# Optimization experiments

Hardware: AMD Instinct MI355X
Metric: run time of the kernel (lower is better)

## Reference

```python
import jax, jax.numpy as jnp
import numpy as np

S = 2048        # seqlen (prefill)
DIM = 4096      # model dim
NH = 32         # query heads
NKV = 8         # kv heads (GQA)
HD = 128        # head dim
SW = 4096       # sliding window / cache length
SCALE = HD ** (-0.5)
NEG = -1e9      # finite -inf for additive mask


def _rope(x, cos, sin):
    # x: (S, H, HD); cos/sin: (S, HD//2). Interleaved even/odd rotation.
    c = cos[:, None, :]
    s = sin[:, None, :]
    x1 = x[..., 0::2]
    x2 = x[..., 1::2]
    pe = jnp.stack([x1 * c - x2 * s, x1 * s + x2 * c], axis=-1)  # (S,H,HD/2,2)
    return pe.reshape(x.shape).astype(x.dtype)


def setup_inputs() -> dict:
    key = jax.random.key(0)
    kx, kq, kk, kv, ko = jax.random.split(key, 5)
    sd = 1.0 / np.sqrt(DIM)
    x = jax.random.normal(kx, (S, DIM), dtype=jnp.float32)
    wq = jax.random.normal(kq, (NH * HD, DIM), dtype=jnp.float32) * sd
    wk = jax.random.normal(kk, (NKV * HD, DIM), dtype=jnp.float32) * sd
    wv = jax.random.normal(kv, (NKV * HD, DIM), dtype=jnp.float32) * sd
    wo = jax.random.normal(ko, (DIM, NH * HD), dtype=jnp.float32) * (1.0 / np.sqrt(NH * HD))
    # RoPE tables
    inv_freq = 1.0 / (10000.0 ** (np.arange(0, HD, 2, dtype=np.float32) / HD))  # (HD/2,)
    t = np.arange(S, dtype=np.float32)
    freqs = np.outer(t, inv_freq)  # (S, HD/2)
    cos_freq = jnp.asarray(np.cos(freqs), dtype=jnp.float32)
    sin_freq = jnp.asarray(np.sin(freqs), dtype=jnp.float32)
    # sliding-window causal additive mask
    i = jnp.arange(S)[:, None]
    j = jnp.arange(S)[None, :]
    allowed = (j <= i) & ((i - j) < SW)
    mask = jnp.where(allowed, 0.0, NEG).astype(jnp.float32)
    cache_k = jnp.zeros((SW, NKV, HD), dtype=jnp.float32)
    cache_v = jnp.zeros((SW, NKV, HD), dtype=jnp.float32)
    positions = jnp.arange(S, dtype=jnp.int32)
    return {"x": x, "cos_freq": cos_freq, "sin_freq": sin_freq, "mask": mask,
            "wq": wq, "wk": wk, "wv": wv, "wo": wo,
            "cache_k": cache_k, "cache_v": cache_v, "positions": positions}


def reference(x, cos_freq, sin_freq, mask, wq, wk, wv, wo, cache_k, cache_v, positions):
    seqlen = x.shape[0]
    kv_repeats = NH // NKV
    # QKV projections (eqx.nn.Linear: y = x @ W.T)
    xq = (x @ wq.T).reshape(seqlen, NH, HD)
    xk = (x @ wk.T).reshape(seqlen, NKV, HD)
    xv = (x @ wv.T).reshape(seqlen, NKV, HD)
    # RoPE on q and k (offset 0)
    xq = _rope(xq, cos_freq, sin_freq)
    xk = _rope(xk, cos_freq, sin_freq)
    # KV-cache scatter update
    cache_k = cache_k.at[positions].set(xk[positions])
    cache_v = cache_v.at[positions].set(xv[positions])
    # prefill path: GQA head repeat
    key_ = jnp.repeat(xk, kv_repeats, axis=1)   # (S, NH, HD)
    val_ = jnp.repeat(xv, kv_repeats, axis=1)
    # explicit matmul-softmax-matmul attention, heads leading
    q = jnp.transpose(xq, (1, 0, 2))            # (NH, S, HD)
    k = jnp.transpose(key_, (1, 0, 2))
    v = jnp.transpose(val_, (1, 0, 2))
    scores = jnp.einsum('hqd,hkd->hqk', q, k) * SCALE
    scores = scores + mask[None, ...]
    probs = jax.nn.softmax(scores.astype(jnp.float32), axis=-1).astype(q.dtype)
    out = jnp.einsum('hqk,hkd->hqd', probs, v)  # (NH, S, HD)
    out = jnp.transpose(out, (1, 0, 2)).reshape(seqlen, NH * HD)
    out = out @ wo.T
    return (out, cache_k, cache_v)
```

## Files before the change

kernel.cpp:

```cpp
#include <hip/hip_runtime.h>
#include <stdint.h>

#define S_LEN 2048
#define DIM_   4096
#define NH_    32
#define NKV_   8
#define HD_    128
#define QK_SCALE 0.08838834764831845f

typedef __attribute__((ext_vector_type(8)))  short  s16x8;
typedef __attribute__((ext_vector_type(4)))  float  f32x4;
typedef __attribute__((ext_vector_type(16))) float  f32x16;
typedef __attribute__((ext_vector_type(8))) unsigned short u16x8;
typedef __attribute__((ext_vector_type(4))) unsigned short u16x4;

union frag_u { s16x8 f; uint32_t w[4]; };

__device__ __forceinline__ unsigned short f2bf(float f) {
  union { float f; uint32_t u; } v; v.f = f;
  return (unsigned short)((v.u + 0x7fffu + ((v.u >> 16) & 1u)) >> 16);
}

__device__ __forceinline__ uint32_t cvt_pk_bf16(float lo, float hi2) {
  uint32_t r;
  asm volatile("v_cvt_pk_bf16_f32 %0, %1, %2" : "=v"(r) : "v"(lo), "v"(hi2));
  return r;
}

__device__ __forceinline__ void async_cp16(const void* g, void* l) {
  __builtin_amdgcn_global_load_lds(
      (const __attribute__((address_space(1))) unsigned int*)g,
      (__attribute__((address_space(3))) unsigned int*)l, 16, 0, 0);
}

#define WAITV(n) asm volatile("s_waitcnt vmcnt(" #n ")" ::: "memory")

__global__ __launch_bounds__(256) void cast_f32_bf16(
    const float* __restrict__ src, unsigned short* __restrict__ dst, int n4) {
  const int i = blockIdx.x * 256 + threadIdx.x;
  if (i >= n4) return;
  const float4 v = ((const float4*)src)[i];
  u16x4 o; o[0] = f2bf(v.x); o[1] = f2bf(v.y); o[2] = f2bf(v.z); o[3] = f2bf(v.w);
  ((u16x4*)dst)[i] = o;
}

template <int NT, int NTILE_N, int NCF, int NBCH>
__global__ __launch_bounds__(512, 4) void gemmF(
    const unsigned short* __restrict__ A, const unsigned short* __restrict__ B,
    float* __restrict__ C, int ldc) {
  constexpr int BUFB = 16384 + NTILE_N * 128;
  __shared__ unsigned char lds[2 * BUFB];

  const int bid = blockIdx.x;
  const int idx = (bid & 7) * 64 + (bid >> 3);
  const int m = idx & 15, n = idx >> 4;
  const int m0 = m * 128, n0 = n * NTILE_N;

  const int tid = threadIdx.x;
  const int wave = tid >> 6, lane = tid & 63;
  const int wm = wave >> 2, wn = wave & 3;
  const int fr = lane & 15, g = lane >> 4;

  int offA[2][2], offB[NCF][2];
#pragma unroll
  for (int rf = 0; rf < 2; ++rf)
#pragma unroll
    for (int kk = 0; kk < 2; ++kk)
      offA[rf][kk] = (wm * 32 + rf * 16 + fr) * 128 + (((kk * 4 + g + fr) & 7) << 4);
#pragma unroll
  for (int cf = 0; cf < NCF; ++cf)
#pragma unroll
    for (int kk = 0; kk < 2; ++kk)
      offB[cf][kk] = (wn * NCF * 16 + cf * 16 + fr) * 128 + (((kk * 4 + g + fr) & 7) << 4);

  const int srk = (((tid & 7) - (tid >> 3)) & 7) * 8;
  uint32_t aoff[2];
  uint32_t boff[NBCH];
#pragma unroll
  for (int h = 0; h < 2; ++h)
    aoff[h] = (uint32_t)((m0 + h * 64 + (tid >> 3)) * 4096 + srk);
#pragma unroll
  for (int i = 0; i < NBCH; ++i)
    boff[i] = (uint32_t)((n0 + i * 64 + (tid >> 3)) * 4096 + srk);

  f32x4 acc[2][2][NCF] = {};
  s16x8 fa[2][2], fb[NCF][2];

#define STGA(H, T, BUF)                                                       \
  async_cp16(A + aoff[H] + (size_t)(T) * 64,                                  \
             (char*)lds + (BUF) * BUFB + (H) * 8192 + tid * 16);
#define STGB(T, BUF)                                                          \
  { _Pragma("unroll") for (int i_ = 0; i_ < NBCH; ++i_)                       \
      async_cp16(B + boff[i_] + (size_t)(T) * 64,                             \
                 (char*)lds + (BUF) * BUFB + 16384 + i_ * 8192 + tid * 16); }
#define LDA(AA, P)                                                            \
  { _Pragma("unroll") for (int rf = 0; rf < 2; ++rf)                          \
      _Pragma("unroll") for (int kk = 0; kk < 2; ++kk)                        \
        fa[rf][kk] = *(const s16x8*)((char*)lds + (P) * BUFB +                \
                                     (AA) * 8192 + offA[rf][kk]); }
#define LDBF(P)                                                               \
  { _Pragma("unroll") for (int cf = 0; cf < NCF; ++cf)                        \
      _Pragma("unroll") for (int kk = 0; kk < 2; ++kk)                        \
        fb[cf][kk] = *(const s16x8*)((char*)lds + (P) * BUFB + 16384 +        \
                                     offB[cf][kk]); }
#define BARLG()                                                               \
  __builtin_amdgcn_s_barrier();                                               \
  asm volatile("s_waitcnt lgkmcnt(0)" ::: "memory");                          \
  __builtin_amdgcn_sched_barrier(0);
#define MF(AA)                                                                \
  __builtin_amdgcn_s_setprio(1);                                              \
  { _Pragma("unroll") for (int kk = 0; kk < 2; ++kk)                          \
      _Pragma("unroll") for (int rf = 0; rf < 2; ++rf)                        \
        _Pragma("unroll") for (int cf = 0; cf < NCF; ++cf)                    \
          acc[AA][rf][cf] = __builtin_amdgcn_mfma_f32_16x16x32_bf16(          \
              fa[rf][kk], fb[cf][kk], acc[AA][rf][cf], 0, 0, 0); }            \
  __builtin_amdgcn_s_setprio(0);
#define GATEN do { if constexpr (NBCH == 3) { WAITV(4); } else { WAITV(3); } } while (0)

#define GROUPF(J, P, DO1, DO2, GATE)                                          \
  {                                                                           \
    LDA(0, P); LDBF(P);                                                       \
    if (DO1) { STGA(1, (J) + 1, (P) ^ 1); }                                   \
    BARLG(); MF(0);                                                           \
    __builtin_amdgcn_s_barrier();                                             \
    LDA(1, P);                                                                \
    if (DO2) { STGA(0, (J) + 2, P); STGB((J) + 2, P); }                       \
    BARLG(); MF(1);                                                           \
    GATE;                                                                     \
    __builtin_amdgcn_s_barrier();                                             \
  }

  STGA(0, 0, 0); STGB(0, 0); STGA(1, 0, 0);
  STGA(0, 1, 1); STGB(1, 1);
  GATEN;
  __builtin_amdgcn_s_barrier();

  for (int j = 0; j + 3 < NT; j += 2) {
    GROUPF(j, 0, true, true, GATEN);
    GROUPF(j + 1, 1, true, true, GATEN);
  }
  GROUPF(NT - 2, 0, true, false, WAITV(0));
  GROUPF(NT - 1, 1, false, false, );

#pragma unroll
  for (int AA = 0; AA < 2; ++AA)
#pragma unroll
    for (int rf = 0; rf < 2; ++rf)
#pragma unroll
      for (int cf = 0; cf < NCF; ++cf) {
        float* cp = C + (size_t)(m0 + AA * 64 + wm * 32 + rf * 16 + g * 4) * ldc
                      + (n0 + wn * NCF * 16 + cf * 16 + fr);
#pragma unroll
        for (int r = 0; r < 4; ++r) cp[(size_t)r * ldc] = acc[AA][rf][cf][r];
      }
#undef STGA
#undef STGB
#undef LDA
#undef LDBF
#undef BARLG
#undef MF
#undef GATEN
#undef GROUPF
}

__global__ __launch_bounds__(256) void rope_q_kern(
    const float* __restrict__ xqkv, const float* __restrict__ cos_f,
    const float* __restrict__ sin_f, unsigned short* __restrict__ qb) {
  const int gid = blockIdx.x * 256 + threadIdx.x;
  const int e0 = gid * 8;
  const int s = e0 >> 12;
  const int col = e0 & 4095;
  const int i0 = (col & 127) >> 1;
  const float* src = xqkv + (size_t)s * 6144 + col;
  const float4 f1 = *(const float4*)src;
  const float4 f2 = *(const float4*)(src + 4);
  const float4 c  = *(const float4*)(cos_f + s * 64 + i0);
  const float4 sn = *(const float4*)(sin_f + s * 64 + i0);
  u16x8 o;
  o[0] = f2bf((f1.x * c.x - f1.y * sn.x) * QK_SCALE);
  o[1] = f2bf((f1.x * sn.x + f1.y * c.x) * QK_SCALE);
  o[2] = f2bf((f1.z * c.y - f1.w * sn.y) * QK_SCALE);
  o[3] = f2bf((f1.z * sn.y + f1.w * c.y) * QK_SCALE);
  o[4] = f2bf((f2.x * c.z - f2.y * sn.z) * QK_SCALE);
  o[5] = f2bf((f2.x * sn.z + f2.y * c.z) * QK_SCALE);
  o[6] = f2bf((f2.z * c.w - f2.w * sn.w) * QK_SCALE);
  o[7] = f2bf((f2.z * sn.w + f2.w * c.w) * QK_SCALE);
  *(u16x8*)(qb + e0) = o;
}

__global__ __launch_bounds__(256) void rope_k_kern(
    const float* __restrict__ xqkv, const float* __restrict__ cos_f,
    const float* __restrict__ sin_f, float* __restrict__ ck, unsigned short* __restrict__ kb) {
  const int gid = blockIdx.x * 256 + threadIdx.x;
  const int e0 = gid * 8;
  const int s = e0 >> 10;
  const int col = e0 & 1023;
  const int i0 = (col & 127) >> 1;
  const float* src = xqkv + (size_t)s * 6144 + 4096 + col;
  const float4 f1 = *(const float4*)src;
  const float4 f2 = *(const float4*)(src + 4);
  const float4 c  = *(const float4*)(cos_f + s * 64 + i0);
  const float4 sn = *(const float4*)(sin_f + s * 64 + i0);
  const float r0 = f1.x * c.x - f1.y * sn.x, r1 = f1.x * sn.x + f1.y * c.x;
  const float r2 = f1.z * c.y - f1.w * sn.y, r3 = f1.z * sn.y + f1.w * c.y;
  const float r4 = f2.x * c.z - f2.y * sn.z, r5 = f2.x * sn.z + f2.y * c.z;
  const float r6 = f2.z * c.w - f2.w * sn.w, r7 = f2.z * sn.w + f2.w * c.w;
  float4 o1; o1.x = r0; o1.y = r1; o1.z = r2; o1.w = r3;
  float4 o2; o2.x = r4; o2.y = r5; o2.z = r6; o2.w = r7;
  *(float4*)(ck + (size_t)s * 1024 + col) = o1;
  *(float4*)(ck + (size_t)s * 1024 + col + 4) = o2;
  u16x8 o;
  o[0] = f2bf(r0); o[1] = f2bf(r1); o[2] = f2bf(r2); o[3] = f2bf(r3);
  o[4] = f2bf(r4); o[5] = f2bf(r5); o[6] = f2bf(r6); o[7] = f2bf(r7);
  *(u16x8*)(kb + (size_t)s * 1024 + col) = o;
}

__global__ __launch_bounds__(256) void vtrans_kern(
    const float* __restrict__ xqkv, float* __restrict__ cv, unsigned short* __restrict__ vtb) {
  __shared__ float tile[64][65];
  const int st = blockIdx.x * 64;
  const int ct = blockIdx.y * 64;
  const int tid = threadIdx.x;
#pragma unroll
  for (int j = 0; j < 16; ++j) {
    const int lin = tid + j * 256;
    const int si = lin >> 6, ci = lin & 63;
    const float v = xqkv[(size_t)(st + si) * 6144 + 5120 + ct + ci];
    cv[(size_t)(st + si) * 1024 + ct + ci] = v;
    tile[si][ci] = v;
  }
  __syncthreads();
#pragma unroll
  for (int j = 0; j < 16; ++j) {
    const int lin = tid + j * 256;
    const int co = lin >> 6, so = lin & 63;
    vtb[(size_t)(ct + co) * 2048 + st + so] = f2bf(tile[so][co]);
  }
}

__global__ __launch_bounds__(256, 2) void attn_fwd2(
    const unsigned short* __restrict__ qb, const unsigned short* __restrict__ kb,
    const unsigned short* __restrict__ vtb, unsigned short* __restrict__ ob) {
  __shared__ unsigned short Ks[2][64 * 128];
  __shared__ unsigned short Vs[2][128 * 64];
  const int bx = blockIdx.x;
  const int h  = blockIdx.y;
  const int hkv = h >> 2;
  const int g = (bx & 1) ? (15 - (bx >> 1)) : (bx >> 1);
  const int qtile = (h < 16) ? g : (15 - g);
  const int q0 = qtile * 128;
  const int tid = threadIdx.x, wave = tid >> 6, lane = tid & 63;
  const int col = lane & 31;
  const int hi  = lane >> 5;
  const int q0w = q0 + wave * 32;
  const int nt = (q0 >> 6) + 2;

  s16x8 qf[8];
  {
    const unsigned short* qrow = qb + (size_t)(q0w + col) * 4096 + h * 128 + hi * 8;
#pragma unroll
    for (int ks = 0; ks < 8; ++ks) qf[ks] = *(const s16x8*)(qrow + ks * 16);
  }

  f32x16 oacc[4] = {};
  float m_s = -3e30f, l_s = 0.0f;

#define STAGE_K(KT, B)                                                        \
  {                                                                           \
    const unsigned short* src = kb + (size_t)((KT) * 64) * 1024 + hkv * 128;  \
    _Pragma("unroll")                                                         \
    for (int i_ = 0; i_ < 4; ++i_) {                                          \
      const int c_ = wave * 4 + i_;                                           \
      const int row_ = c_ * 4 + (lane >> 4);                                  \
      const int cb_ = ((lane & 15) * 16) ^ ((row_ & 7) << 4);                 \
      async_cp16(src + (size_t)row_ * 1024 + (cb_ >> 1), (char*)Ks[B] + c_ * 1024); \
    }                                                                         \
  }
#define STAGE_V(KT, B)                                                        \
  {                                                                           \
    const unsigned short* src = vtb + (size_t)hkv * (128 * 2048) + (KT) * 64; \
    _Pragma("unroll")                                                         \
    for (int i_ = 0; i_ < 4; ++i_) {                                          \
      const int c_ = wave * 4 + i_;                                           \
      const int row_ = c_ * 8 + (lane >> 3);                                  \
      const int cb_ = ((lane & 7) * 16) ^ ((row_ & 7) << 4);                  \
      async_cp16(src + (size_t)row_ * 2048 + (cb_ >> 1), (char*)Vs[B] + c_ * 1024); \
    }                                                                         \
  }

  STAGE_K(0, 0); STAGE_V(0, 0);
  __syncthreads();

  for (int kt = 0; kt < nt; ++kt) {
    const int kv0 = kt * 64;
    const int cur = kt & 1;
    if (kt + 1 < nt) { STAGE_K(kt + 1, cur ^ 1); STAGE_V(kt + 1, cur ^ 1); }

    if (kv0 < q0w + 32) {
      f32x16 s0 = {}, s1 = {};
#pragma unroll
      for (int ks = 0; ks < 8; ++ks) {
        const int gcb = 32 * ks + 16 * hi;
        const int sw = (col & 7) << 4;
        const s16x8 k0 = *(const s16x8*)((const char*)Ks[cur] + col * 256 + (gcb ^ sw));
        const s16x8 k1 = *(const s16x8*)((const char*)Ks[cur] + (32 + col) * 256 + (gcb ^ sw));
        s0 = __builtin_amdgcn_mfma_f32_32x32x16_bf16(k0, qf[ks], s0, 0, 0, 0);
        s1 = __builtin_amdgcn_mfma_f32_32x32x16_bf16(k1, qf[ks], s1, 0, 0, 0);
      }

      const int qg = q0w + col;
      if (kv0 + 63 > q0w) {
#pragma unroll
        for (int r = 0; r < 16; ++r) {
          const int kvl = (r & 3) + 8 * (r >> 2) + 4 * hi;
          if (kv0 + kvl > qg)      s0[r] = -3e30f;
          if (kv0 + 32 + kvl > qg) s1[r] = -3e30f;
        }
      }

      float mxl = s0[0];
#pragma unroll
      for (int r = 1; r < 16; ++r) mxl = fmaxf(mxl, s0[r]);
#pragma unroll
      for (int r = 0; r < 16; ++r) mxl = fmaxf(mxl, s1[r]);
      const float mxf = fmaxf(mxl, __shfl_xor(mxl, 32));
      if (__any(mxf > m_s + 8.0f)) {
        const float mn = fmaxf(m_s, mxf);
        const float scl = __expf(m_s - mn);
        m_s = mn;
        l_s *= scl;
#pragma unroll
        for (int r = 0; r < 16; ++r) {
          const int qq = (r & 3) + 8 * (r >> 2) + 4 * hi;
          const float sr = __int_as_float(
              __builtin_amdgcn_ds_bpermute(qq * 4, __float_as_int(scl)));
          oacc[0][r] *= sr; oacc[1][r] *= sr; oacc[2][r] *= sr; oacc[3][r] *= sr;
        }
      }
      float lsum = 0.0f;
#pragma unroll
      for (int r = 0; r < 16; ++r) {
        s0[r] = __expf(s0[r] - m_s); s1[r] = __expf(s1[r] - m_s);
        lsum += s0[r] + s1[r];
      }
      lsum += __shfl_xor(lsum, 32);
      l_s += lsum;

#define PV_STEP(KS, PP)                                                       \
      {                                                                       \
        const int rb2 = 8 * ((KS) & 1);                                       \
        const uint32_t g0a = cvt_pk_bf16(PP[rb2 + 0], PP[rb2 + 1]);           \
        const uint32_t g0b = cvt_pk_bf16(PP[rb2 + 2], PP[rb2 + 3]);           \
        const uint32_t g1a = cvt_pk_bf16(PP[rb2 + 4], PP[rb2 + 5]);           \
        const uint32_t g1b = cvt_pk_bf16(PP[rb2 + 6], PP[rb2 + 7]);           \
        const uint32_t sa = hi ? g0a : g1a, sb = hi ? g0b : g1b;              \
        const uint32_t ra = (uint32_t)__shfl_xor((int)sa, 32);                \
        const uint32_t rb_ = (uint32_t)__shfl_xor((int)sb, 32);               \
        frag_u af;                                                            \
        af.w[0] = hi ? ra  : g0a; af.w[1] = hi ? rb_ : g0b;                   \
        af.w[2] = hi ? g1a : ra;  af.w[3] = hi ? g1b : rb_;                   \
        const int gcb = 32 * (KS) + 16 * hi;                                  \
        const int vsw = (col & 7) << 4;                                       \
        _Pragma("unroll")                                                     \
        for (int db = 0; db < 4; ++db) {                                      \
          const s16x8 bv = *(const s16x8*)((const char*)Vs[cur] +             \
              (db * 32 + col) * 128 + (gcb ^ vsw));                           \
          oacc[db] = __builtin_amdgcn_mfma_f32_32x32x16_bf16(af.f, bv, oacc[db], 0, 0, 0); \
        }                                                                     \
      }
      PV_STEP(0, s0); PV_STEP(1, s0); PV_STEP(2, s1); PV_STEP(3, s1);
#undef PV_STEP
    }
    __syncthreads();
  }

  const float linv = 1.0f / l_s;
#pragma unroll
  for (int r = 0; r < 16; ++r) {
    const int qq = (r & 3) + 8 * (r >> 2) + 4 * hi;
    const float lr = __int_as_float(
        __builtin_amdgcn_ds_bpermute(qq * 4, __float_as_int(linv)));
    unsigned short* orow = ob + (size_t)(q0w + qq) * 4096 + h * 128 + col;
#pragma unroll
    for (int db = 0; db < 4; ++db)
      orow[db * 32] = f2bf(oacc[db][r] * lr);
  }
#undef STAGE_K
#undef STAGE_V
}

extern "C" void kernel_launch(void* const* d_in, const int* in_sizes, int n_in,
                              void* d_out, int out_size, void* d_ws, size_t ws_size,
                              hipStream_t stream) {
  const float* x     = (const float*)d_in[0];
  const float* cos_f = (const float*)d_in[1];
  const float* sin_f = (const float*)d_in[2];
  const float* wq = (const float*)d_in[4];
  const float* wk = (const float*)d_in[5];
  const float* wv = (const float*)d_in[6];
  const float* wo = (const float*)d_in[7];
  float* out = (float*)d_out;

  char* ws = (char*)d_ws;
  unsigned short* xb    = (unsigned short*)(ws);
  unsigned short* wqkvb = (unsigned short*)(ws + 16777216);
  unsigned short* wob   = (unsigned short*)(ws + 67108864);
  float*          xqkv  = (float*)(ws + 100663296);
  unsigned short* qb    = (unsigned short*)(ws + 150994944);
  unsigned short* kb    = (unsigned short*)(ws + 167772160);
  unsigned short* vtb   = (unsigned short*)(ws + 171966464);
  unsigned short* attno = (unsigned short*)(ws + 176160768);

  cast_f32_bf16<<<dim3(8192), 256, 0, stream>>>(x, xb, 2097152);
  cast_f32_bf16<<<dim3(16384), 256, 0, stream>>>(wq, wqkvb, 4194304);
  cast_f32_bf16<<<dim3(4096), 256, 0, stream>>>(wk, wqkvb + 16777216, 1048576);
  cast_f32_bf16<<<dim3(4096), 256, 0, stream>>>(wv, wqkvb + 20971520, 1048576);
  cast_f32_bf16<<<dim3(16384), 256, 0, stream>>>(wo, wob, 4194304);

  gemmF<64, 192, 3, 3><<<dim3(512), 512, 0, stream>>>(xb, wqkvb, xqkv, 6144);

  rope_q_kern<<<dim3(4096), 256, 0, stream>>>(xqkv, cos_f, sin_f, qb);
  rope_k_kern<<<dim3(1024), 256, 0, stream>>>(xqkv, cos_f, sin_f, out + 8388608, kb);
  vtrans_kern<<<dim3(32, 16), 256, 0, stream>>>(xqkv, out + 12582912, vtb);

  (void)hipMemsetAsync(out + 10485760, 0, 8388608, stream);
  (void)hipMemsetAsync(out + 14680064, 0, 8388608, stream);

  attn_fwd2<<<dim3(16, 32), 256, 0, stream>>>(qb, kb, vtb, attno);

  gemmF<64, 128, 2, 2><<<dim3(512), 512, 0, stream>>>(attno, wob, out, 4096);
}
```

Before: 317.7 us.

## Restructure GEMM to 4 waves with larger per-wave tiles and reordered staging

The bf16 GEMM goes from 8 waves per 512-thread block to 4 waves per 256-thread block. Each wave now computes a 64-row by NCF*16-column tile, loading four A fragments and streaming B fragments one k-slice at a time. The async staging order changes so B for the next tile is issued in the first half-step and A for tile j+2 in the second. The aim is more MFMA work per LDS fragment load and fewer waves contending at barriers, at the cost of higher register pressure (a 4x6 accumulator grid for the QKV GEMM) and less latency hiding per CU.

```diff
diff --git a/kernel.cpp b/kernel.cpp
--- a/kernel.cpp
+++ b/kernel.cpp
@@ -45,7 +45,7 @@
 }
 
 template <int NT, int NTILE_N, int NCF, int NBCH>
-__global__ __launch_bounds__(512, 4) void gemmF(
+__global__ __launch_bounds__(256, 2) void gemmF(
     const unsigned short* __restrict__ A, const unsigned short* __restrict__ B,
     float* __restrict__ C, int ldc) {
   constexpr int BUFB = 16384 + NTILE_N * 128;
@@ -58,15 +58,15 @@
 
   const int tid = threadIdx.x;
   const int wave = tid >> 6, lane = tid & 63;
-  const int wm = wave >> 2, wn = wave & 3;
+  const int wm = wave >> 1, wn = wave & 1;
   const int fr = lane & 15, g = lane >> 4;
 
-  int offA[2][2], offB[NCF][2];
-#pragma unroll
-  for (int rf = 0; rf < 2; ++rf)
+  int offA[4][2], offB[NCF][2];
+#pragma unroll
+  for (int rf = 0; rf < 4; ++rf)
 #pragma unroll
     for (int kk = 0; kk < 2; ++kk)
-      offA[rf][kk] = (wm * 32 + rf * 16 + fr) * 128 + (((kk * 4 + g + fr) & 7) << 4);
+      offA[rf][kk] = wm * 8192 + (rf * 16 + fr) * 128 + (((kk * 4 + g + fr) & 7) << 4);
 #pragma unroll
   for (int cf = 0; cf < NCF; ++cf)
 #pragma unroll
@@ -74,92 +74,87 @@
       offB[cf][kk] = (wn * NCF * 16 + cf * 16 + fr) * 128 + (((kk * 4 + g + fr) & 7) << 4);
 
   const int srk = (((tid & 7) - (tid >> 3)) & 7) * 8;
-  uint32_t aoff[2];
+  uint32_t aoff[2][2];
   uint32_t boff[NBCH];
 #pragma unroll
   for (int h = 0; h < 2; ++h)
-    aoff[h] = (uint32_t)((m0 + h * 64 + (tid >> 3)) * 4096 + srk);
+#pragma unroll
+    for (int i = 0; i < 2; ++i)
+      aoff[h][i] = (uint32_t)((m0 + h * 64 + i * 32 + (tid >> 3)) * 4096 + srk);
 #pragma unroll
   for (int i = 0; i < NBCH; ++i)
-    boff[i] = (uint32_t)((n0 + i * 64 + (tid >> 3)) * 4096 + srk);
-
-  f32x4 acc[2][2][NCF] = {};
-  s16x8 fa[2][2], fb[NCF][2];
-
-#define STGA(H, T, BUF)                                                       \
-  async_cp16(A + aoff[H] + (size_t)(T) * 64,                                  \
-             (char*)lds + (BUF) * BUFB + (H) * 8192 + tid * 16);
+    boff[i] = (uint32_t)((n0 + i * 32 + (tid >> 3)) * 4096 + srk);
+
+  f32x4 acc[4][NCF] = {};
+  s16x8 fa[4][2], fbk[NCF];
+
+#define STGA(T, BUF)                                                          \
+  { _Pragma("unroll") for (int h_ = 0; h_ < 2; ++h_)                          \
+      _Pragma("unroll") for (int i_ = 0; i_ < 2; ++i_)                        \
+        async_cp16(A + aoff[h_][i_] + (size_t)(T) * 64,                       \
+                   (char*)lds + (BUF) * BUFB + h_ * 8192 + i_ * 4096 + tid * 16); }
 #define STGB(T, BUF)                                                          \
   { _Pragma("unroll") for (int i_ = 0; i_ < NBCH; ++i_)                       \
       async_cp16(B + boff[i_] + (size_t)(T) * 64,                             \
-                 (char*)lds + (BUF) * BUFB + 16384 + i_ * 8192 + tid * 16); }
-#define LDA(AA, P)                                                            \
-  { _Pragma("unroll") for (int rf = 0; rf < 2; ++rf)                          \
+                 (char*)lds + (BUF) * BUFB + 16384 + i_ * 4096 + tid * 16); }
+#define LDA2(P)                                                               \
+  { _Pragma("unroll") for (int rf = 0; rf < 4; ++rf)                          \
       _Pragma("unroll") for (int kk = 0; kk < 2; ++kk)                        \
-        fa[rf][kk] = *(const s16x8*)((char*)lds + (P) * BUFB +                \
-                                     (AA) * 8192 + offA[rf][kk]); }
-#define LDBF(P)                                                               \
+        fa[rf][kk] = *(const s16x8*)((char*)lds + (P) * BUFB + offA[rf][kk]); }
+#define LDBK(KK, P)                                                           \
   { _Pragma("unroll") for (int cf = 0; cf < NCF; ++cf)                        \
-      _Pragma("unroll") for (int kk = 0; kk < 2; ++kk)                        \
-        fb[cf][kk] = *(const s16x8*)((char*)lds + (P) * BUFB + 16384 +        \
-                                     offB[cf][kk]); }
+      fbk[cf] = *(const s16x8*)((char*)lds + (P) * BUFB + 16384 + offB[cf][KK]); }
 #define BARLG()                                                               \
   __builtin_amdgcn_s_barrier();                                               \
   asm volatile("s_waitcnt lgkmcnt(0)" ::: "memory");                          \
   __builtin_amdgcn_sched_barrier(0);
-#define MF(AA)                                                                \
+#define MFK(KK)                                                               \
   __builtin_amdgcn_s_setprio(1);                                              \
-  { _Pragma("unroll") for (int kk = 0; kk < 2; ++kk)                          \
-      _Pragma("unroll") for (int rf = 0; rf < 2; ++rf)                        \
-        _Pragma("unroll") for (int cf = 0; cf < NCF; ++cf)                    \
-          acc[AA][rf][cf] = __builtin_amdgcn_mfma_f32_16x16x32_bf16(          \
-              fa[rf][kk], fb[cf][kk], acc[AA][rf][cf], 0, 0, 0); }            \
+  { _Pragma("unroll") for (int rf = 0; rf < 4; ++rf)                          \
+      _Pragma("unroll") for (int cf = 0; cf < NCF; ++cf)                      \
+        acc[rf][cf] = __builtin_amdgcn_mfma_f32_16x16x32_bf16(                \
+            fa[rf][KK], fbk[cf], acc[rf][cf], 0, 0, 0); }                     \
   __builtin_amdgcn_s_setprio(0);
-#define GATEN do { if constexpr (NBCH == 3) { WAITV(4); } else { WAITV(3); } } while (0)
 
 #define GROUPF(J, P, DO1, DO2, GATE)                                          \
   {                                                                           \
-    LDA(0, P); LDBF(P);                                                       \
-    if (DO1) { STGA(1, (J) + 1, (P) ^ 1); }                                   \
-    BARLG(); MF(0);                                                           \
+    LDA2(P); LDBK(0, P);                                                      \
+    if (DO1) { STGB((J) + 1, (P) ^ 1); }                                      \
+    BARLG(); MFK(0);                                                          \
     __builtin_amdgcn_s_barrier();                                             \
-    LDA(1, P);                                                                \
-    if (DO2) { STGA(0, (J) + 2, P); STGB((J) + 2, P); }                       \
-    BARLG(); MF(1);                                                           \
+    LDBK(1, P);                                                               \
+    if (DO2) { STGA((J) + 2, P); }                                            \
+    BARLG(); MFK(1);                                                          \
     GATE;                                                                     \
     __builtin_amdgcn_s_barrier();                                             \
   }
 
-  STGA(0, 0, 0); STGB(0, 0); STGA(1, 0, 0);
-  STGA(0, 1, 1); STGB(1, 1);
-  GATEN;
+  STGA(0, 0); STGB(0, 0); STGA(1, 1);
+  WAITV(4);
   __builtin_amdgcn_s_barrier();
 
   for (int j = 0; j + 3 < NT; j += 2) {
-    GROUPF(j, 0, true, true, GATEN);
-    GROUPF(j + 1, 1, true, true, GATEN);
+    GROUPF(j, 0, true, true, WAITV(4));
+    GROUPF(j + 1, 1, true, true, WAITV(4));
   }
   GROUPF(NT - 2, 0, true, false, WAITV(0));
   GROUPF(NT - 1, 1, false, false, );
 
 #pragma unroll
-  for (int AA = 0; AA < 2; ++AA)
-#pragma unroll
-    for (int rf = 0; rf < 2; ++rf)
-#pragma unroll
-      for (int cf = 0; cf < NCF; ++cf) {
-        float* cp = C + (size_t)(m0 + AA * 64 + wm * 32 + rf * 16 + g * 4) * ldc
-                      + (n0 + wn * NCF * 16 + cf * 16 + fr);
-#pragma unroll
-        for (int r = 0; r < 4; ++r) cp[(size_t)r * ldc] = acc[AA][rf][cf][r];
-      }
+  for (int rf = 0; rf < 4; ++rf)
+#pragma unroll
+    for (int cf = 0; cf < NCF; ++cf) {
+      float* cp = C + (size_t)(m0 + wm * 64 + rf * 16 + g * 4) * ldc
+                    + (n0 + wn * NCF * 16 + cf * 16 + fr);
+#pragma unroll
+      for (int r = 0; r < 4; ++r) cp[(size_t)r * ldc] = acc[rf][cf][r];
+    }
 #undef STGA
 #undef STGB
-#undef LDA
-#undef LDBF
+#undef LDA2
+#undef LDBK
 #undef BARLG
-#undef MF
-#undef GATEN
+#undef MFK
 #undef GROUPF
 }
 
@@ -417,7 +412,7 @@
   cast_f32_bf16<<<dim3(4096), 256, 0, stream>>>(wv, wqkvb + 20971520, 1048576);
   cast_f32_bf16<<<dim3(16384), 256, 0, stream>>>(wo, wob, 4194304);
 
-  gemmF<64, 192, 3, 3><<<dim3(512), 512, 0, stream>>>(xb, wqkvb, xqkv, 6144);
+  gemmF<64, 192, 6, 6><<<dim3(512), 256, 0, stream>>>(xb, wqkvb, xqkv, 6144);
 
   rope_q_kern<<<dim3(4096), 256, 0, stream>>>(xqkv, cos_f, sin_f, qb);
   rope_k_kern<<<dim3(1024), 256, 0, stream>>>(xqkv, cos_f, sin_f, out + 8388608, kb);
@@ -428,5 +423,5 @@
 
   attn_fwd2<<<dim3(16, 32), 256, 0, stream>>>(qb, kb, vtb, attno);
 
-  gemmF<64, 128, 2, 2><<<dim3(512), 512, 0, stream>>>(attno, wob, out, 4096);
-}
+  gemmF<64, 128, 4, 4><<<dim3(512), 256, 0, stream>>>(attno, wob, out, 4096);
+}
```

Result: no change. 314.0 us (-1.2%).
